# Kernel optimization log

Measured on AMD Instinct MI355X. Metric: run time of the kernel, lower is better.

The kernel has to match this reference:

```python
import jax, jax.numpy as jnp
import numpy as np

RES = 128
SH_DIM = 9            # (deg+1)^2, deg=2
CH = SH_DIM * 3 + 1   # 28: 3*9 SH rgb coeffs + 1 sigma
AABB_MIN = -1.0
AABB_MAX = 1.0
STEP = (AABB_MAX - AABB_MIN) / (RES - 1)   # voxel_len = mean(aabb_size/(res-1))
UNIFORM = 0.5
N_SAMPLES = int(RES * 3 / UNIFORM)         # plenoxels count: 768
EPS = 1e-10


def sh_encode_deg2(d):
    # real spherical harmonics basis, degree 2 (9 coefficients), on normalized dirs
    d = d / jnp.linalg.norm(d, axis=-1, keepdims=True)
    x, y, z = d[..., 0], d[..., 1], d[..., 2]
    C0 = 0.28209479177387814
    C1 = 0.4886025119029199
    C20, C21, C22 = 1.0925484305920792, -1.0925484305920792, 0.31539156525252005
    C23, C24 = -1.0925484305920792, 0.5462742152960396
    return jnp.stack([
        jnp.full_like(x, C0),
        -C1 * y, C1 * z, -C1 * x,
        C20 * x * y, C21 * y * z, C22 * (2.0 * z * z - x * x - y * y),
        C23 * x * z, C24 * (x * x - y * y),
    ], axis=-1)


def grid_sample_3d(grid, pts):
    # grid: [D,H,W,C]; pts: [...,3] in [-1,1], (x,y,z) with x->W, y->H, z->D.
    # Matches torch F.grid_sample(mode='bilinear', padding_mode='zeros', align_corners=True).
    D, H, W, C = grid.shape
    lead = pts.shape[:-1]
    p = pts.reshape(-1, 3)
    x = (p[:, 0] + 1.0) * 0.5 * (W - 1)
    y = (p[:, 1] + 1.0) * 0.5 * (H - 1)
    z = (p[:, 2] + 1.0) * 0.5 * (D - 1)
    x0f, y0f, z0f = jnp.floor(x), jnp.floor(y), jnp.floor(z)
    fx, fy, fz = x - x0f, y - y0f, z - z0f
    x0 = x0f.astype(jnp.int32)
    y0 = y0f.astype(jnp.int32)
    z0 = z0f.astype(jnp.int32)
    flat = grid.reshape(-1, C)
    out = jnp.zeros((p.shape[0], C), grid.dtype)
    for dz in (0, 1):
        for dy in (0, 1):
            for dx in (0, 1):
                xi, yi, zi = x0 + dx, y0 + dy, z0 + dz
                valid = (xi >= 0) & (xi < W) & (yi >= 0) & (yi < H) & (zi >= 0) & (zi < D)
                w = ((fx if dx else 1.0 - fx)
                     * (fy if dy else 1.0 - fy)
                     * (fz if dz else 1.0 - fz)) * valid
                idx = (jnp.clip(zi, 0, D - 1) * H + jnp.clip(yi, 0, H - 1)) * W + jnp.clip(xi, 0, W - 1)
                out = out + w[:, None] * flat[idx]
    return out.reshape(lead + (C,))


def setup_inputs() -> dict:
    key = jax.random.key(0)
    k1, k2, k3 = jax.random.split(key, 3)
    B = 4096
    # origins on a radius-3 sphere, aimed at jittered targets inside the unit box
    o = jax.random.normal(k1, (B, 3), dtype=jnp.float32)
    rays_o = 3.0 * o / jnp.linalg.norm(o, axis=-1, keepdims=True)
    tgt = jax.random.uniform(k2, (B, 3), dtype=jnp.float32, minval=-0.5, maxval=0.5)
    d = tgt - rays_o
    rays_d = d / jnp.linalg.norm(d, axis=-1, keepdims=True)
    grid_data = 0.1 * jax.random.normal(k3, (RES ** 3, CH), dtype=jnp.float32)
    grid_data = grid_data.at[:, -1].add(0.1)  # ini_sigma offset
    return {"rays_d": rays_d, "rays_o": rays_o, "grid_data": grid_data}


def reference(rays_d, rays_o, grid_data):
    B = rays_d.shape[0]
    aabb_lo = jnp.full((3,), AABB_MIN, rays_o.dtype)
    aabb_hi = jnp.full((3,), AABB_MAX, rays_o.dtype)
    # ray-AABB intersection (no_grad in torch)
    t_pos = (aabb_hi - rays_o) / rays_d
    t_neg = (aabb_lo - rays_o) / rays_d
    t_in = jnp.minimum(t_pos, t_neg)
    t_out = jnp.maximum(t_pos, t_neg)
    start = jnp.max(t_in, axis=-1)                  # [B]
    stop = jnp.min(t_out, axis=-1, keepdims=True)   # [B,1]
    # tensor_linspace from start+u*step to start+u*step*n, then clamp max=stop
    w = jnp.linspace(0.0, 1.0, N_SAMPLES, dtype=rays_o.dtype)  # [S]
    s0 = start + UNIFORM * STEP
    s1 = start + UNIFORM * STEP * N_SAMPLES
    intersections = s0[:, None] * (1.0 - w) + s1[:, None] * w   # [B,S]
    intersections = jnp.minimum(intersections, stop)
    t = intersections[:, :-1]                                    # [B,S-1]
    pts = rays_o[:, None, :] + t[:, :, None] * rays_d[:, None, :]
    pts = (pts - AABB_MIN) * (2.0 / (AABB_MAX - AABB_MIN)) - 1.0  # normalize to [-1,1]
    # trilinear sample of the voxel grid (torch layout: D=res0,H=res1,W=res2; x->W)
    interp = grid_sample_3d(grid_data.reshape(RES, RES, RES, CH), pts)  # [B,S-1,CH]
    sigma = interp[..., -1]
    rgb_sh = interp[..., :-1].reshape(B, N_SAMPLES - 1, 3, SH_DIM)
    sh = sh_encode_deg2(rays_d)                                   # [B,9]
    rgb = jnp.einsum('bsck,bk->bsc', rgb_sh, sh)
    # volumetric rendering
    dists = jnp.diff(intersections, axis=1) * jnp.linalg.norm(rays_d, axis=-1, keepdims=True)
    alpha = 1.0 - jnp.exp(-jax.nn.relu(sigma) * dists)
    cum_light = jnp.concatenate(
        [jnp.ones((B, 1), alpha.dtype), jnp.cumprod(1.0 - alpha[:, :-1] + EPS, axis=-1)], axis=-1)
    abs_light = alpha * cum_light
    acc_map = abs_light.sum(-1)
    rgb_map = (abs_light[..., None] * jax.nn.sigmoid(rgb)).sum(-2)
    depth = (abs_light * t).sum(-1)
    rgb_map = rgb_map + (1.0 - acc_map[:, None])  # white background
    return rgb_map, alpha, depth
```

## Files before the change

kernel.cpp:

```cpp
#include <hip/hip_runtime.h>
#include <math.h>

#define RESG 128
#define CHG 28
#define NT 767
#define NLBKT 48

template <int PAT>
static __device__ __forceinline__ float swz(float x) {
    return __int_as_float(__builtin_amdgcn_ds_swizzle(__float_as_int(x), PAT));
}

__global__ __launch_bounds__(1024) void prep_sort(
    const float* __restrict__ rays_d, const float* __restrict__ rays_o,
    int* __restrict__ perm, int B)
{
    __shared__ int cnt[64];
    __shared__ int off[64];
    __shared__ unsigned char keys[4096];
    const int tid = threadIdx.x;
    if (tid < 64) cnt[tid] = 0;
    __syncthreads();
    for (int r = tid; r < B; r += 1024) {
        const float ox = rays_o[r*3+0], oy = rays_o[r*3+1], oz = rays_o[r*3+2];
        const float dx = rays_d[r*3+0], dy = rays_d[r*3+1], dz = rays_d[r*3+2];
        float txp = (1.0f - ox)/dx, txn = (-1.0f - ox)/dx;
        float typ = (1.0f - oy)/dy, tyn = (-1.0f - oy)/dy;
        float tzp = (1.0f - oz)/dz, tzn = (-1.0f - oz)/dz;
        const float start = fmaxf(fmaxf(fminf(txp,txn), fminf(typ,tyn)), fminf(tzp,tzn));
        const float stop  = fminf(fminf(fmaxf(txp,txn), fmaxf(typ,tyn)), fmaxf(tzp,tzn));
        int n_proc = (int)((stop - start) * 127.0f) + 2;
        n_proc = n_proc < 0 ? 0 : (n_proc > NT ? NT : n_proc);
        int lvl = n_proc >> 4; if (lvl > NLBKT-1) lvl = NLBKT-1;
        const int k = (NLBKT-1) - lvl;
        keys[r] = (unsigned char)k;
        atomicAdd(&cnt[k], 1);
    }
    __syncthreads();
    if (tid < 64) {
        int v = cnt[tid];
        int incl = v;
        #pragma unroll
        for (int o2 = 1; o2 < 64; o2 <<= 1) {
            const int n = __shfl_up(incl, o2, 64);
            if ((tid & 63) >= o2) incl += n;
        }
        off[tid] = incl - v;
    }
    __syncthreads();
    for (int r = tid; r < B; r += 1024) {
        const int slot = atomicAdd(&off[keys[r]], 1);
        perm[slot] = r;
    }
}

__global__ __launch_bounds__(256) void nerf_grid_kernel(
    const float* __restrict__ rays_d,
    const float* __restrict__ rays_o,
    const float* __restrict__ grid,
    const int*   __restrict__ perm,
    float* __restrict__ out_rgb,
    float* __restrict__ out_alpha,
    float* __restrict__ out_depth)
{
    const int ray  = perm[blockIdx.x];
    const int tid  = threadIdx.x;
    const int lane = tid & 63;
    const int wave = tid >> 6;

    const float EPSC   = 1e-10f;
    const float INV127 = 1.0f / 127.0f;

    __shared__ float a_lds[NT + 1];
    __shared__ float r_lds[NT + 1];
    __shared__ float g_lds[NT + 1];
    __shared__ float b_lds[NT + 1];
    __shared__ float wprod[4];
    __shared__ float red[4][5];

    const float ox = rays_o[ray*3+0], oy = rays_o[ray*3+1], oz = rays_o[ray*3+2];
    const float dx = rays_d[ray*3+0], dy = rays_d[ray*3+1], dz = rays_d[ray*3+2];
    const float dnorm = sqrtf(dx*dx + dy*dy + dz*dz);

    float txp = (1.0f - ox)/dx, txn = (-1.0f - ox)/dx;
    float typ = (1.0f - oy)/dy, tyn = (-1.0f - oy)/dy;
    float tzp = (1.0f - oz)/dz, tzn = (-1.0f - oz)/dz;
    const float start = fmaxf(fmaxf(fminf(txp,txn), fminf(typ,tyn)), fminf(tzp,tzn));
    const float stop  = fminf(fminf(fmaxf(txp,txn), fmaxf(typ,tyn)), fmaxf(tzp,tzn));

    int n_proc = (int)((stop - start) * 127.0f) + 2;
    n_proc = n_proc < 0 ? 0 : (n_proc > NT ? NT : n_proc);

    const float inv = 1.0f/dnorm;
    const float nx = dx*inv, ny = dy*inv, nz = dz*inv;
    float sh0, sh1, sh2, sh3, sh4, sh5, sh6, sh7, sh8;
    {
        const float C0 = 0.28209479177387814f;
        const float C1 = 0.4886025119029199f;
        const float C20 = 1.0925484305920792f, C21 = -1.0925484305920792f;
        const float C22 = 0.31539156525252005f;
        const float C23 = -1.0925484305920792f, C24 = 0.5462742152960396f;
        sh0 = C0;   sh1 = -C1*ny; sh2 = C1*nz; sh3 = -C1*nx;
        sh4 = C20*nx*ny; sh5 = C21*ny*nz;
        sh6 = C22*(2.0f*nz*nz - nx*nx - ny*ny);
        sh7 = C23*nx*nz; sh8 = C24*(nx*nx - ny*ny);
    }

    const int samp   = lane >> 3;
    const int corner = lane & 7;
    const int cdx = corner & 1, cdy = (corner >> 1) & 1, cdz = corner >> 2;

    for (int base = wave*8; base < n_proc; base += 32) {
        const int s = base + samp;
        float rr = 0.0f, gg = 0.0f, bb = 0.0f, sg = 0.0f;
        float t0 = 0.0f, dist = 0.0f;
        bool live = false;
        if (s < n_proc) {
            t0 = fminf(start + (float)(s+1)*INV127, stop);
            const float t1 = fminf(start + (float)(s+2)*INV127, stop);
            dist = (t1 - t0) * dnorm;
            live = dist > 0.0f;
        }
        if (live) {
            const float gx = (ox + t0*dx + 1.0f)*63.5f;
            const float gy = (oy + t0*dy + 1.0f)*63.5f;
            const float gz = (oz + t0*dz + 1.0f)*63.5f;
            const float fx0 = floorf(gx), fy0 = floorf(gy), fz0 = floorf(gz);
            const float fx = gx - fx0, fy = gy - fy0, fz = gz - fz0;
            const int xi = (int)fx0 + cdx;
            const int yi = (int)fy0 + cdy;
            const int zi = (int)fz0 + cdz;
            const bool valid = ((unsigned)xi < (unsigned)RESG) &
                               ((unsigned)yi < (unsigned)RESG) &
                               ((unsigned)zi < (unsigned)RESG);
            const float w = (cdx ? fx : 1.0f-fx) *
                            (cdy ? fy : 1.0f-fy) *
                            (cdz ? fz : 1.0f-fz);
            if (valid && w != 0.0f) {
                const float4* row = (const float4*)(grid + (size_t)(((zi*RESG) + yi)*RESG + xi)*CHG);
                const float4 v0 = row[0], v1 = row[1], v2 = row[2], v3 = row[3];
                const float4 v4 = row[4], v5 = row[5], v6 = row[6];
                rr = w*(v0.x*sh0 + v0.y*sh1 + v0.z*sh2 + v0.w*sh3 +
                        v1.x*sh4 + v1.y*sh5 + v1.z*sh6 + v1.w*sh7 + v2.x*sh8);
                gg = w*(v2.y*sh0 + v2.z*sh1 + v2.w*sh2 + v3.x*sh3 +
                        v3.y*sh4 + v3.z*sh5 + v3.w*sh6 + v4.x*sh7 + v4.y*sh8);
                bb = w*(v4.z*sh0 + v4.w*sh1 + v5.x*sh2 + v5.y*sh3 +
                        v5.z*sh4 + v5.w*sh5 + v6.x*sh6 + v6.y*sh7 + v6.z*sh8);
                sg = w*v6.w;
            }
        }
        rr += swz<0x041F>(rr); gg += swz<0x041F>(gg); bb += swz<0x041F>(bb); sg += swz<0x041F>(sg);
        rr += swz<0x081F>(rr); gg += swz<0x081F>(gg); bb += swz<0x081F>(bb); sg += swz<0x081F>(sg);
        rr += swz<0x101F>(rr); gg += swz<0x101F>(gg); bb += swz<0x101F>(bb); sg += swz<0x101F>(sg);

        if (corner == 0 && s < n_proc) {
            a_lds[s] = live ? 1.0f - expf(-fmaxf(sg, 0.0f)*dist) : 0.0f;
            r_lds[s] = 1.0f/(1.0f + expf(-rr));
            g_lds[s] = 1.0f/(1.0f + expf(-gg));
            b_lds[s] = 1.0f/(1.0f + expf(-bb));
        }
    }
    __syncthreads();

    for (int s = tid; s < NT; s += 256)
        out_alpha[(size_t)ray*NT + s] = (s < n_proc) ? a_lds[s] : 0.0f;

    float a_r[3], q_r[3], t_r[3], rr_r[3], gg_r[3], bb_r[3];
    #pragma unroll
    for (int k = 0; k < 3; ++k) {
        const int s = tid*3 + k;
        float a = 0.0f, rr = 0.0f, gg = 0.0f, bb = 0.0f, tt = 0.0f;
        if (s < NT) {
            tt = fminf(start + (float)(s+1)*INV127, stop);
            if (s < n_proc) {
                a = a_lds[s];
                rr = r_lds[s]; gg = g_lds[s]; bb = b_lds[s];
            }
        }
        a_r[k] = a; q_r[k] = (s < NT) ? (1.0f - a + EPSC) : 1.0f;
        t_r[k] = tt; rr_r[k] = rr; gg_r[k] = gg; bb_r[k] = bb;
    }

    const float P = q_r[0]*q_r[1]*q_r[2];
    float incl = P;
    #pragma unroll
    for (int off2 = 1; off2 < 64; off2 <<= 1) {
        const float n = __shfl_up(incl, off2, 64);
        if (lane >= off2) incl *= n;
    }
    float excl = __shfl_up(incl, 1, 64);
    if (lane == 0) excl = 1.0f;

    if (lane == 63) wprod[wave] = incl;
    __syncthreads();
    float wpre = 1.0f;
    for (int w2 = 0; w2 < 4; ++w2) if (w2 < wave) wpre *= wprod[w2];

    float cum = wpre * excl;
    float accA = 0.0f, accR = 0.0f, accG = 0.0f, accB = 0.0f, accD = 0.0f;
    #pragma unroll
    for (int k = 0; k < 3; ++k) {
        const float abs_l = a_r[k] * cum;
        accA += abs_l;
        accR += abs_l * rr_r[k];
        accG += abs_l * gg_r[k];
        accB += abs_l * bb_r[k];
        accD += abs_l * t_r[k];
        cum *= q_r[k];
    }

    #pragma unroll
    for (int off2 = 32; off2 > 0; off2 >>= 1) {
        accA += __shfl_down(accA, off2, 64);
        accR += __shfl_down(accR, off2, 64);
        accG += __shfl_down(accG, off2, 64);
        accB += __shfl_down(accB, off2, 64);
        accD += __shfl_down(accD, off2, 64);
    }
    if (lane == 0) {
        red[wave][0] = accA; red[wave][1] = accR; red[wave][2] = accG;
        red[wave][3] = accB; red[wave][4] = accD;
    }
    __syncthreads();
    if (tid == 0) {
        float A = 0.0f, R = 0.0f, G = 0.0f, Bv = 0.0f, D = 0.0f;
        #pragma unroll
        for (int w2 = 0; w2 < 4; ++w2) {
            A += red[w2][0]; R += red[w2][1]; G += red[w2][2];
            Bv += red[w2][3]; D += red[w2][4];
        }
        const float bg = 1.0f - A;
        out_rgb[ray*3+0] = R  + bg;
        out_rgb[ray*3+1] = G  + bg;
        out_rgb[ray*3+2] = Bv + bg;
        out_depth[ray] = D;
    }
}

extern "C" void kernel_launch(void* const* d_in, const int* in_sizes, int n_in,
                              void* d_out, int out_size, void* d_ws, size_t ws_size,
                              hipStream_t stream) {
    const float* rays_d = (const float*)d_in[0];
    const float* rays_o = (const float*)d_in[1];
    const float* grid   = (const float*)d_in[2];
    const int B = in_sizes[0] / 3;

    float* out       = (float*)d_out;
    float* out_rgb   = out;
    float* out_alpha = out + (size_t)B*3;
    float* out_depth = out + (size_t)B*3 + (size_t)B*NT;

    int* perm = (int*)d_ws;

    prep_sort<<<1, 1024, 0, stream>>>(rays_d, rays_o, perm, B);
    nerf_grid_kernel<<<B, 256, 0, stream>>>(rays_d, rays_o, grid, perm,
                                            out_rgb, out_alpha, out_depth);
}
```

Before: 83.33 us.

## Split voxel channels across lanes so each lane trilinearly blends one float4 chunk

Result: slower. 87.56 us (+5.1%).

```diff
diff --git a/kernel.cpp b/kernel.cpp
--- a/kernel.cpp
+++ b/kernel.cpp
@@ -75,6 +75,7 @@
     __shared__ float r_lds[NT + 1];
     __shared__ float g_lds[NT + 1];
     __shared__ float b_lds[NT + 1];
+    __shared__ float sh_lds[12];
     __shared__ float wprod[4];
     __shared__ float red[4][5];
 
@@ -93,68 +94,98 @@
 
     const float inv = 1.0f/dnorm;
     const float nx = dx*inv, ny = dy*inv, nz = dz*inv;
-    float sh0, sh1, sh2, sh3, sh4, sh5, sh6, sh7, sh8;
     {
         const float C0 = 0.28209479177387814f;
         const float C1 = 0.4886025119029199f;
         const float C20 = 1.0925484305920792f, C21 = -1.0925484305920792f;
         const float C22 = 0.31539156525252005f;
         const float C23 = -1.0925484305920792f, C24 = 0.5462742152960396f;
-        sh0 = C0;   sh1 = -C1*ny; sh2 = C1*nz; sh3 = -C1*nx;
-        sh4 = C20*nx*ny; sh5 = C21*ny*nz;
-        sh6 = C22*(2.0f*nz*nz - nx*nx - ny*ny);
-        sh7 = C23*nx*nz; sh8 = C24*(nx*nx - ny*ny);
-    }
-
-    const int samp   = lane >> 3;
-    const int corner = lane & 7;
-    const int cdx = corner & 1, cdy = (corner >> 1) & 1, cdz = corner >> 2;
+        if (tid == 0) {
+            sh_lds[0] = C0;
+            sh_lds[1] = -C1*ny;
+            sh_lds[2] =  C1*nz;
+            sh_lds[3] = -C1*nx;
+            sh_lds[4] = C20*nx*ny;
+            sh_lds[5] = C21*ny*nz;
+            sh_lds[6] = C22*(2.0f*nz*nz - nx*nx - ny*ny);
+            sh_lds[7] = C23*nx*nz;
+            sh_lds[8] = C24*(nx*nx - ny*ny);
+            sh_lds[9] = 0.0f; sh_lds[10] = 0.0f; sh_lds[11] = 0.0f;
+        }
+    }
+    __syncthreads();
+
+    const int samp = lane >> 3;
+    const int j    = lane & 7;
+    float cR[4], cG[4], cB[4];
+    #pragma unroll
+    for (int m = 0; m < 4; ++m) {
+        const int ch = 4*j + m;
+        const int iR = ch      > 11 ? 11 : ch;
+        const int iG = (ch-9)  < 0 ? 0 : ((ch-9)  > 11 ? 11 : (ch-9));
+        const int iB = (ch-18) < 0 ? 0 : ((ch-18) > 11 ? 11 : (ch-18));
+        cR[m] = (ch < 9)               ? sh_lds[iR] : 0.0f;
+        cG[m] = (ch >= 9 && ch < 18)   ? sh_lds[iG] : 0.0f;
+        cB[m] = (ch >= 18 && ch < 27)  ? sh_lds[iB] : 0.0f;
+    }
+    const float cS3 = (j == 6) ? 1.0f : 0.0f;
+    const int chunk_off = (j < 7 ? j : 6) << 4;
+    const char* gridc = (const char*)grid;
 
     for (int base = wave*8; base < n_proc; base += 32) {
         const int s = base + samp;
-        float rr = 0.0f, gg = 0.0f, bb = 0.0f, sg = 0.0f;
-        float t0 = 0.0f, dist = 0.0f;
-        bool live = false;
-        if (s < n_proc) {
-            t0 = fminf(start + (float)(s+1)*INV127, stop);
-            const float t1 = fminf(start + (float)(s+2)*INV127, stop);
-            dist = (t1 - t0) * dnorm;
-            live = dist > 0.0f;
-        }
-        if (live) {
-            const float gx = (ox + t0*dx + 1.0f)*63.5f;
-            const float gy = (oy + t0*dy + 1.0f)*63.5f;
-            const float gz = (oz + t0*dz + 1.0f)*63.5f;
-            const float fx0 = floorf(gx), fy0 = floorf(gy), fz0 = floorf(gz);
-            const float fx = gx - fx0, fy = gy - fy0, fz = gz - fz0;
-            const int xi = (int)fx0 + cdx;
-            const int yi = (int)fy0 + cdy;
-            const int zi = (int)fz0 + cdz;
-            const bool valid = ((unsigned)xi < (unsigned)RESG) &
-                               ((unsigned)yi < (unsigned)RESG) &
-                               ((unsigned)zi < (unsigned)RESG);
-            const float w = (cdx ? fx : 1.0f-fx) *
-                            (cdy ? fy : 1.0f-fy) *
-                            (cdz ? fz : 1.0f-fz);
-            if (valid && w != 0.0f) {
-                const float4* row = (const float4*)(grid + (size_t)(((zi*RESG) + yi)*RESG + xi)*CHG);
-                const float4 v0 = row[0], v1 = row[1], v2 = row[2], v3 = row[3];
-                const float4 v4 = row[4], v5 = row[5], v6 = row[6];
-                rr = w*(v0.x*sh0 + v0.y*sh1 + v0.z*sh2 + v0.w*sh3 +
-                        v1.x*sh4 + v1.y*sh5 + v1.z*sh6 + v1.w*sh7 + v2.x*sh8);
-                gg = w*(v2.y*sh0 + v2.z*sh1 + v2.w*sh2 + v3.x*sh3 +
-                        v3.y*sh4 + v3.z*sh5 + v3.w*sh6 + v4.x*sh7 + v4.y*sh8);
-                bb = w*(v4.z*sh0 + v4.w*sh1 + v5.x*sh2 + v5.y*sh3 +
-                        v5.z*sh4 + v5.w*sh5 + v6.x*sh6 + v6.y*sh7 + v6.z*sh8);
-                sg = w*v6.w;
-            }
-        }
+        const float t0 = fminf(start + (float)(s+1)*INV127, stop);
+        const float t1 = fminf(start + (float)(s+2)*INV127, stop);
+        const float dist = (t1 - t0) * dnorm;
+        const bool live = (s < n_proc) && (dist > 0.0f);
+
+        const float gx = fminf(fmaxf((ox + t0*dx + 1.0f)*63.5f, 0.0f), 127.0f);
+        const float gy = fminf(fmaxf((oy + t0*dy + 1.0f)*63.5f, 0.0f), 127.0f);
+        const float gz = fminf(fmaxf((oz + t0*dz + 1.0f)*63.5f, 0.0f), 127.0f);
+        const float fx0 = floorf(gx), fy0 = floorf(gy), fz0 = floorf(gz);
+        const float fx = gx - fx0, fy = gy - fy0, fz = gz - fz0;
+        const int ix = (int)fx0, iy = (int)fy0, iz = (int)fz0;
+
+        const int Bv = ((iz*RESG + iy)*RESG + ix)*112 + chunk_off;
+        const int offx = (ix < RESG-1) ? 112 : 0;
+        const int offy = (iy < RESG-1) ? 112*RESG : 0;
+        const int offz = (iz < RESG-1) ? 112*RESG*RESG : 0;
+        int offs[8];
+        offs[0] = 0;           offs[1] = offx;
+        offs[2] = offy;        offs[3] = offx + offy;
+        offs[4] = offz;        offs[5] = offz + offx;
+        offs[6] = offz + offy; offs[7] = offz + offx + offy;
+
+        const float liveF = live ? 1.0f : 0.0f;
+        const float wx1 = fx, wx0 = 1.0f - fx;
+        const float wy1 = fy, wy0 = 1.0f - fy;
+        const float wz1 = fz*liveF, wz0 = (1.0f - fz)*liveF;
+        const float w00 = wx0*wy0, w10 = wx1*wy0, w01 = wx0*wy1, w11 = wx1*wy1;
+        float wc[8];
+        wc[0] = w00*wz0; wc[1] = w10*wz0; wc[2] = w01*wz0; wc[3] = w11*wz0;
+        wc[4] = w00*wz1; wc[5] = w10*wz1; wc[6] = w01*wz1; wc[7] = w11*wz1;
+
+        float av0 = 0.0f, av1 = 0.0f, av2 = 0.0f, av3 = 0.0f;
+        #pragma unroll
+        for (int i = 0; i < 8; ++i) {
+            const float4 v = *(const float4*)(gridc + (size_t)(unsigned)(Bv + offs[i]));
+            av0 = fmaf(wc[i], v.x, av0);
+            av1 = fmaf(wc[i], v.y, av1);
+            av2 = fmaf(wc[i], v.z, av2);
+            av3 = fmaf(wc[i], v.w, av3);
+        }
+
+        float rr = av0*cR[0] + av1*cR[1] + av2*cR[2] + av3*cR[3];
+        float gg = av0*cG[0] + av1*cG[1] + av2*cG[2] + av3*cG[3];
+        float bb = av0*cB[0] + av1*cB[1] + av2*cB[2] + av3*cB[3];
+        float sg = av3*cS3;
+
         rr += swz<0x041F>(rr); gg += swz<0x041F>(gg); bb += swz<0x041F>(bb); sg += swz<0x041F>(sg);
         rr += swz<0x081F>(rr); gg += swz<0x081F>(gg); bb += swz<0x081F>(bb); sg += swz<0x081F>(sg);
         rr += swz<0x101F>(rr); gg += swz<0x101F>(gg); bb += swz<0x101F>(bb); sg += swz<0x101F>(sg);
 
-        if (corner == 0 && s < n_proc) {
-            a_lds[s] = live ? 1.0f - expf(-fmaxf(sg, 0.0f)*dist) : 0.0f;
+        if (j == 0 && s < n_proc) {
+            a_lds[s] = 1.0f - expf(-fmaxf(sg, 0.0f)*dist);
             r_lds[s] = 1.0f/(1.0f + expf(-rr));
             g_lds[s] = 1.0f/(1.0f + expf(-gg));
             b_lds[s] = 1.0f/(1.0f + expf(-bb));
@@ -223,16 +254,16 @@
     }
     __syncthreads();
     if (tid == 0) {
-        float A = 0.0f, R = 0.0f, G = 0.0f, Bv = 0.0f, D = 0.0f;
+        float A = 0.0f, R = 0.0f, G = 0.0f, Bv2 = 0.0f, D = 0.0f;
         #pragma unroll
         for (int w2 = 0; w2 < 4; ++w2) {
             A += red[w2][0]; R += red[w2][1]; G += red[w2][2];
-            Bv += red[w2][3]; D += red[w2][4];
+            Bv2 += red[w2][3]; D += red[w2][4];
         }
         const float bg = 1.0f - A;
-        out_rgb[ray*3+0] = R  + bg;
-        out_rgb[ray*3+1] = G  + bg;
-        out_rgb[ray*3+2] = Bv + bg;
+        out_rgb[ray*3+0] = R   + bg;
+        out_rgb[ray*3+1] = G   + bg;
+        out_rgb[ray*3+2] = Bv2 + bg;
         out_depth[ray] = D;
     }
 }
```

## Sort rays by entry cell and direction octant, interleave across XCDs, use fast math

Applied to the files above, without the earlier changes.

Measured after the change: 85.31 us. +2.4%, slower.

```diff
diff --git a/kernel.cpp b/kernel.cpp
--- a/kernel.cpp
+++ b/kernel.cpp
@@ -4,7 +4,7 @@
 #define RESG 128
 #define CHG 28
 #define NT 767
-#define NLBKT 48
+#define NKEY 512
 
 template <int PAT>
 static __device__ __forceinline__ float swz(float x) {
@@ -15,11 +15,12 @@
     const float* __restrict__ rays_d, const float* __restrict__ rays_o,
     int* __restrict__ perm, int B)
 {
-    __shared__ int cnt[64];
-    __shared__ int off[64];
-    __shared__ unsigned char keys[4096];
+    __shared__ int cnt[NKEY];
+    __shared__ int off[NKEY];
+    __shared__ unsigned short keys[4096];
+    __shared__ int sorted_l[4096];
     const int tid = threadIdx.x;
-    if (tid < 64) cnt[tid] = 0;
+    for (int i = tid; i < NKEY; i += 1024) cnt[i] = 0;
     __syncthreads();
     for (int r = tid; r < B; r += 1024) {
         const float ox = rays_o[r*3+0], oy = rays_o[r*3+1], oz = rays_o[r*3+2];
@@ -28,29 +29,36 @@
         float typ = (1.0f - oy)/dy, tyn = (-1.0f - oy)/dy;
         float tzp = (1.0f - oz)/dz, tzn = (-1.0f - oz)/dz;
         const float start = fmaxf(fmaxf(fminf(txp,txn), fminf(typ,tyn)), fminf(tzp,tzn));
-        const float stop  = fminf(fminf(fmaxf(txp,txn), fmaxf(typ,tyn)), fmaxf(tzp,tzn));
-        int n_proc = (int)((stop - start) * 127.0f) + 2;
-        n_proc = n_proc < 0 ? 0 : (n_proc > NT ? NT : n_proc);
-        int lvl = n_proc >> 4; if (lvl > NLBKT-1) lvl = NLBKT-1;
-        const int k = (NLBKT-1) - lvl;
-        keys[r] = (unsigned char)k;
+        const float pex = ox + start*dx, pey = oy + start*dy, pez = oz + start*dz;
+        int ex = (int)fminf(fmaxf((pex + 1.0f)*2.0f, 0.0f), 3.0f);
+        int ey = (int)fminf(fmaxf((pey + 1.0f)*2.0f, 0.0f), 3.0f);
+        int ez = (int)fminf(fmaxf((pez + 1.0f)*2.0f, 0.0f), 3.0f);
+        const int oct = ((dx < 0.f) ? 1 : 0) | ((dy < 0.f) ? 2 : 0) | ((dz < 0.f) ? 4 : 0);
+        const int k = ((ex << 7) | (ey << 5) | (ez << 3) | oct) & (NKEY - 1);
+        keys[r] = (unsigned short)k;
         atomicAdd(&cnt[k], 1);
     }
     __syncthreads();
-    if (tid < 64) {
-        int v = cnt[tid];
-        int incl = v;
-        #pragma unroll
-        for (int o2 = 1; o2 < 64; o2 <<= 1) {
-            const int n = __shfl_up(incl, o2, 64);
-            if ((tid & 63) >= o2) incl += n;
-        }
-        off[tid] = incl - v;
-    }
+    if (tid < NKEY) off[tid] = cnt[tid];
+    __syncthreads();
+    for (int d = 1; d < NKEY; d <<= 1) {
+        int v = 0;
+        if (tid < NKEY && tid >= d) v = off[tid - d];
+        __syncthreads();
+        if (tid < NKEY && tid >= d) off[tid] += v;
+        __syncthreads();
+    }
+    if (tid < NKEY) off[tid] -= cnt[tid];
     __syncthreads();
     for (int r = tid; r < B; r += 1024) {
         const int slot = atomicAdd(&off[keys[r]], 1);
-        perm[slot] = r;
+        sorted_l[slot] = r;
+    }
+    __syncthreads();
+    const int cpx = B >> 3;
+    for (int i = tid; i < B; i += 1024) {
+        const int src = (B & 7) ? i : ((i & 7) * cpx + (i >> 3));
+        perm[i] = sorted_l[src];
     }
 }
 
@@ -116,8 +124,8 @@
         float t0 = 0.0f, dist = 0.0f;
         bool live = false;
         if (s < n_proc) {
-            t0 = fminf(start + (float)(s+1)*INV127, stop);
-            const float t1 = fminf(start + (float)(s+2)*INV127, stop);
+            t0 = fminf(fmaf((float)(s+1), INV127, start), stop);
+            const float t1 = fminf(fmaf((float)(s+2), INV127, start), stop);
             dist = (t1 - t0) * dnorm;
             live = dist > 0.0f;
         }
@@ -154,10 +162,10 @@
         rr += swz<0x101F>(rr); gg += swz<0x101F>(gg); bb += swz<0x101F>(bb); sg += swz<0x101F>(sg);
 
         if (corner == 0 && s < n_proc) {
-            a_lds[s] = live ? 1.0f - expf(-fmaxf(sg, 0.0f)*dist) : 0.0f;
-            r_lds[s] = 1.0f/(1.0f + expf(-rr));
-            g_lds[s] = 1.0f/(1.0f + expf(-gg));
-            b_lds[s] = 1.0f/(1.0f + expf(-bb));
+            a_lds[s] = live ? (1.0f - __expf(-fmaxf(sg, 0.0f)*dist)) : 0.0f;
+            r_lds[s] = __builtin_amdgcn_rcpf(1.0f + __expf(-rr));
+            g_lds[s] = __builtin_amdgcn_rcpf(1.0f + __expf(-gg));
+            b_lds[s] = __builtin_amdgcn_rcpf(1.0f + __expf(-bb));
         }
     }
     __syncthreads();
@@ -171,7 +179,7 @@
         const int s = tid*3 + k;
         float a = 0.0f, rr = 0.0f, gg = 0.0f, bb = 0.0f, tt = 0.0f;
         if (s < NT) {
-            tt = fminf(start + (float)(s+1)*INV127, stop);
+            tt = fminf(fmaf((float)(s+1), INV127, start), stop);
             if (s < n_proc) {
                 a = a_lds[s];
                 rr = r_lds[s]; gg = g_lds[s]; bb = b_lds[s];
```
